# Kernel optimization log

Hardware: AMD Instinct MI355X
Metric: run time of the kernel (lower is better)

## Reference

```python
import jax, jax.numpy as jnp
import numpy as np
import math

QK = 32
IN_DIM = 64
TEXT_DIM = 256


def setup_inputs() -> dict:
    key = jax.random.key(0)
    ks = jax.random.split(key, 12)
    B, C, D, H, W = 2, IN_DIM, 32, 96, 96
    x = jax.random.normal(ks[0], (B, C, D, H, W), dtype=jnp.float32)
    text_emb = jax.random.normal(ks[1], (32, TEXT_DIM), dtype=jnp.float32)
    s = 0.05
    wq = jax.random.normal(ks[2], (QK, C), dtype=jnp.float32) * s
    bq = jax.random.normal(ks[3], (QK,), dtype=jnp.float32) * s
    wk = jax.random.normal(ks[4], (QK, C), dtype=jnp.float32) * s
    bk = jax.random.normal(ks[5], (QK,), dtype=jnp.float32) * s
    wv = jax.random.normal(ks[6], (C, C), dtype=jnp.float32) * s
    bv = jax.random.normal(ks[7], (C,), dtype=jnp.float32) * s
    wt = jax.random.normal(ks[8], (QK, TEXT_DIM), dtype=jnp.float32) * s
    bt = jax.random.normal(ks[9], (QK,), dtype=jnp.float32) * s
    pos_embed = jax.random.normal(ks[10], (1, QK, D, 1, 1), dtype=jnp.float32) * s
    gamma = jax.random.normal(ks[11], (1,), dtype=jnp.float32) * s
    return {"x": x, "text_emb": text_emb, "wq": wq, "bq": bq, "wk": wk,
            "bk": bk, "wv": wv, "bv": bv, "wt": wt, "bt": bt,
            "pos_embed": pos_embed, "gamma": gamma}


def _conv1x1(w, b, x):
    # 1x1x1 Conv3d == channel-mixing matmul: (O,C) x (B,C,D,H,W) -> (B,O,D,H,W)
    return jnp.einsum('oc,bcdhw->bodhw', w, x) + b[None, :, None, None, None]


def reference(x, text_emb, wq, bq, wk, bk, wv, bv, wt, bt, pos_embed, gamma):
    B, C, D, H, W = x.shape
    # text bias: Linear then mean over tokens -> (qk,)
    text_bias = (text_emb @ wt.T + bt).mean(axis=0)
    tb = text_bias[None, :, None, None, None]
    Q = _conv1x1(wq, bq, x) + pos_embed + tb  # (B,qk,D,H,W)
    K = _conv1x1(wk, bk, x) + pos_embed + tb
    V = _conv1x1(wv, bv, x)                   # (B,C,D,H,W)
    scale = math.sqrt(QK)
    # axial attention along D, independent per (b,h,w)
    scores = jnp.einsum('bqdhw,bqehw->bhwde', Q, K) / scale
    attn = jax.nn.softmax(scores, axis=-1)    # (B,H,W,D,D)
    out = jnp.einsum('bhwde,bcehw->bcdhw', attn, V)
    g = jax.nn.sigmoid(gamma[0])
    return g * out + (1.0 - g) * x
```

## Files before the change

kernel.cpp:

```cpp
#include <hip/hip_runtime.h>
#include <hip/hip_bf16.h>

#define B_   2
#define C_   64
#define D_   32
#define H_   96
#define W_   96
#define QK_  32
#define TW_  8
#define HW_  (H_*W_)
#define DHW_ (D_*H_*W_)
#define TDIM_ 256

#define WS_PB   0
#define WS_KB2  1024
#define WS_WQP  2048
#define WS_WKP  3072
#define WS_WVP  4096
#define WS_PBT  6144
#define WS_KBT  7168

typedef __attribute__((ext_vector_type(8))) short short8;
typedef __attribute__((ext_vector_type(4))) float f32x4;

__device__ __forceinline__ uint packbf2(float lo, float hi) {
    uint a = (uint)__bfloat16_as_ushort(__float2bfloat16(lo));
    uint b = (uint)__bfloat16_as_ushort(__float2bfloat16(hi));
    return a | (b << 16);
}

__global__ void prep_kernel(const float* __restrict__ te,
                            const float* __restrict__ wt,
                            const float* __restrict__ bt,
                            const float* __restrict__ bq,
                            const float* __restrict__ bk,
                            const float* __restrict__ wq,
                            const float* __restrict__ wk,
                            const float* __restrict__ wv,
                            const float* __restrict__ pos,
                            float* __restrict__ ws) {
    __shared__ float tm[TDIM_];
    __shared__ float qtb[QK_], ktb[QK_];
    const int t = threadIdx.x;
    float s = 0.f;
    #pragma unroll
    for (int tok = 0; tok < 32; ++tok) s += te[tok*TDIM_ + t];
    tm[t] = s * (1.0f/32.0f);
    __syncthreads();
    if (t < QK_) {
        float acc = bt[t];
        for (int c = 0; c < TDIM_; ++c) acc += wt[t*TDIM_ + c] * tm[c];
        qtb[t] = bq[t] + acc;
        ktb[t] = bk[t] + acc;
    }
    __syncthreads();
    for (int i = t; i < 1024; i += TDIM_) {
        int q = i >> 5, dd = i & 31;
        ws[WS_PB  + i] = qtb[q] + pos[q*32 + dd];
        ws[WS_KB2 + i] = ktb[q] + pos[q*32 + dd];
    }
    for (int i = t; i < 1024; i += TDIM_) {
        int dd = i >> 5, q = i & 31;
        ws[WS_PBT + i] = qtb[q] + pos[q*32 + dd];
        ws[WS_KBT + i] = ktb[q] + pos[q*32 + dd];
    }
    uint* wsu = reinterpret_cast<uint*>(ws);
    for (int i = t; i < 1024; i += TDIM_) {
        int q = i >> 5, cp = i & 31;
        wsu[WS_WQP + i] = packbf2(wq[q*64 + 2*cp], wq[q*64 + 2*cp + 1]);
    }
    for (int i = t; i < 1024; i += TDIM_) {
        int q = i >> 5, cp = i & 31;
        wsu[WS_WKP + i] = packbf2(wk[q*64 + 2*cp], wk[q*64 + 2*cp + 1]);
    }
    for (int i = t; i < 2048; i += TDIM_) {
        int c = i >> 5, cp = i & 31;
        wsu[WS_WVP + i] = packbf2(wv[c*64 + 2*cp], wv[c*64 + 2*cp + 1]);
    }
}

__global__ __launch_bounds__(256, 2)
void attn_main(const float* __restrict__ x,
               const float* __restrict__ bv,
               const float* __restrict__ gm,
               const float* __restrict__ ws,
               float* __restrict__ out) {
    __shared__ uint lds[20480];
    uint* const R_X  = lds;
    uint* const R_QS = lds + 8192;
    uint* const R_KS = lds + 12288;
    uint* const R_V  = lds + 8192;
    uint* const R_AP = lds + 16384;
    uint* const R_O  = lds;

    const uint*  wsu = reinterpret_cast<const uint*>(ws);
    const uint*  wqp = wsu + WS_WQP;
    const uint*  wkp = wsu + WS_WKP;
    const uint*  wvp = wsu + WS_WVP;
    const float* PBT = ws + WS_PBT;
    const float* KBT = ws + WS_KBT;

    const int tid  = threadIdx.x;
    const int lane = tid & 63;
    const int wid  = tid >> 6;
    const int ln   = lane & 15;
    const int lg   = lane >> 4;
    const int d    = tid >> 3;
    const int w    = tid & 7;

    const int bx  = blockIdx.x;
    const int r8  = bx & 7;
    const int q2  = (bx >> 3) & 3;
    const int G   = bx >> 5;
    const int wp_ = G % 3;
    const int hh  = (G / 3) % 12;
    const int b   = G / 36;
    const int h   = hh*8 + r8;
    const int wtile = wp_*4 + q2;

    const int base = b*(C_*DHW_) + d*HW_ + h*W_ + wtile*TW_ + w;

    uint xp[32];
    {
        float xv[64];
        #pragma unroll
        for (int c = 0; c < 64; ++c) xv[c] = x[base + c*DHW_];
        const int key = tid & 7;
        #pragma unroll
        for (int j = 0; j < 8; ++j) {
            uint4 pk;
            pk.x = packbf2(xv[8*j+0], xv[8*j+1]);
            pk.y = packbf2(xv[8*j+2], xv[8*j+3]);
            pk.z = packbf2(xv[8*j+4], xv[8*j+5]);
            pk.w = packbf2(xv[8*j+6], xv[8*j+7]);
            xp[4*j+0] = pk.x; xp[4*j+1] = pk.y;
            xp[4*j+2] = pk.z; xp[4*j+3] = pk.w;
            *reinterpret_cast<uint4*>(R_X + tid*32 + (((j ^ key) & 7) << 2)) = pk;
        }
    }
    __syncthreads();

    {
        uint4 Af[4][2];
        #pragma unroll
        for (int mt = 0; mt < 4; ++mt) {
            const uint* tab = (mt < 2) ? wqp : wkp;
            const int qrow = 16*(mt & 1) + ln;
            #pragma unroll
            for (int kt = 0; kt < 2; ++kt)
                Af[mt][kt] = *reinterpret_cast<const uint4*>(tab + qrow*32 + 16*kt + 4*lg);
        }
        #pragma unroll
        for (int nt = 0; nt < 4; ++nt) {
            const int pos = 16*(4*wid + nt) + ln;
            const int dd  = pos >> 3;
            short8 Bf[2];
            #pragma unroll
            for (int kt = 0; kt < 2; ++kt) {
                uint4 raw = *reinterpret_cast<const uint4*>(
                    R_X + pos*32 + ((((4*kt + lg) ^ (pos & 7)) & 7) << 2));
                Bf[kt] = __builtin_bit_cast(short8, raw);
            }
            #pragma unroll
            for (int mt = 0; mt < 4; ++mt) {
                const float* bt_ = (mt < 2) ? PBT : KBT;
                f32x4 acc = *reinterpret_cast<const f32x4*>(bt_ + dd*32 + 16*(mt & 1) + 4*lg);
                #pragma unroll
                for (int kt = 0; kt < 2; ++kt)
                    acc = __builtin_amdgcn_mfma_f32_16x16x32_bf16(
                        __builtin_bit_cast(short8, Af[mt][kt]), Bf[kt], acc, 0, 0, 0);
                uint p0 = packbf2(acc[0], acc[1]);
                uint p1 = packbf2(acc[2], acc[3]);
                uint* dst = (mt < 2) ? R_QS : R_KS;
                const int s4  = 2*(mt & 1) + (lg >> 1);
                const int off = (((s4 ^ (dd & 3)) & 3) << 2) + 2*(lg & 1);
                *reinterpret_cast<uint2*>(dst + pos*16 + off) = make_uint2(p0, p1);
            }
        }
    }
    __syncthreads();

    {
        const float rsc = 0.17677669529663687f;
        #pragma unroll
        for (int pp = 0; pp < 2; ++pp) {
            const int wp = 2*wid + pp;
            short8 Aq[2], Bk[2];
            #pragma unroll
            for (int t2 = 0; t2 < 2; ++t2) {
                const int row = (16*t2 + ln)*8 + wp;
                const int off = (((lg ^ (ln & 3)) & 3) << 2);
                uint4 rq = *reinterpret_cast<const uint4*>(R_QS + row*16 + off);
                uint4 rk = *reinterpret_cast<const uint4*>(R_KS + row*16 + off);
                Aq[t2] = __builtin_bit_cast(short8, rq);
                Bk[t2] = __builtin_bit_cast(short8, rk);
            }
            f32x4 sc[2][2];
            #pragma unroll
            for (int mtS = 0; mtS < 2; ++mtS)
                #pragma unroll
                for (int ntS = 0; ntS < 2; ++ntS) {
                    f32x4 z = {0.f, 0.f, 0.f, 0.f};
                    sc[mtS][ntS] = __builtin_amdgcn_mfma_f32_16x16x32_bf16(
                        Aq[mtS], Bk[ntS], z, 0, 0, 0);
                }
            #pragma unroll
            for (int mtS = 0; mtS < 2; ++mtS) {
                #pragma unroll
                for (int r2 = 0; r2 < 4; ++r2) {
                    float m = fmaxf(sc[mtS][0][r2], sc[mtS][1][r2]);
                    #pragma unroll
                    for (int sh = 1; sh <= 8; sh <<= 1) m = fmaxf(m, __shfl_xor(m, sh));
                    float p0 = __expf((sc[mtS][0][r2] - m) * rsc);
                    float p1 = __expf((sc[mtS][1][r2] - m) * rsc);
                    float sm = p0 + p1;
                    #pragma unroll
                    for (int sh = 1; sh <= 8; sh <<= 1) sm += __shfl_xor(sm, sh);
                    const float rs = 1.0f / sm;
                    p0 *= rs; p1 *= rs;
                    const float q0 = __shfl_xor(p0, 1);
                    const float q1 = __shfl_xor(p1, 1);
                    if ((lane & 1) == 0) {
                        const int dd2 = 16*mtS + 4*lg + r2;
                        const int u_  = ln >> 1;
                        const int rowb = (dd2*8 + wp)*16;
                        {
                            const int s3  = (u_ >> 2);
                            const int off = (((s3 ^ (dd2 & 3)) & 3) << 2) + (u_ & 3);
                            R_AP[rowb + off] = packbf2(p0, q0);
                        }
                        {
                            const int s3  = 2 + (u_ >> 2);
                            const int off = (((s3 ^ (dd2 & 3)) & 3) << 2) + (u_ & 3);
                            R_AP[rowb + off] = packbf2(p1, q1);
                        }
                    }
                }
            }
        }
    }
    __syncthreads();

    {
        short8 Bf[4][2];
        #pragma unroll
        for (int nt = 0; nt < 4; ++nt) {
            const int pos = 16*(4*wid + nt) + ln;
            #pragma unroll
            for (int kt = 0; kt < 2; ++kt) {
                uint4 raw = *reinterpret_cast<const uint4*>(
                    R_X + pos*32 + ((((4*kt + lg) ^ (pos & 7)) & 7) << 2));
                Bf[nt][kt] = __builtin_bit_cast(short8, raw);
            }
        }
        #pragma unroll
        for (int mt = 0; mt < 4; ++mt) {
            short8 Av[2];
            #pragma unroll
            for (int kt = 0; kt < 2; ++kt) {
                uint4 raw = *reinterpret_cast<const uint4*>(wvp + (16*mt + ln)*32 + 16*kt + 4*lg);
                Av[kt] = __builtin_bit_cast(short8, raw);
            }
            const f32x4 bini = *reinterpret_cast<const f32x4*>(bv + 16*mt + 4*lg);
            f32x4 a4[4];
            #pragma unroll
            for (int nt = 0; nt < 4; ++nt) {
                a4[nt] = bini;
                #pragma unroll
                for (int kt = 0; kt < 2; ++kt)
                    a4[nt] = __builtin_amdgcn_mfma_f32_16x16x32_bf16(Av[kt], Bf[nt][kt], a4[nt], 0, 0, 0);
            }
            #pragma unroll
            for (int r2 = 0; r2 < 4; ++r2) {
                uint u0, u1, u2, u3;
                { float o = a4[0][r2]; float p = __shfl_xor(o, 8); u0 = packbf2(o, p); }
                { float o = a4[1][r2]; float p = __shfl_xor(o, 8); u1 = packbf2(o, p); }
                { float o = a4[2][r2]; float p = __shfl_xor(o, 8); u2 = packbf2(o, p); }
                { float o = a4[3][r2]; float p = __shfl_xor(o, 8); u3 = packbf2(o, p); }
                if ((lane & 8) == 0) {
                    const int c   = 16*mt + 4*lg + r2;
                    const int wv_ = lane & 7;
                    const int phys = (wid ^ lg ^ (wv_ & 3)) & 3;
                    *reinterpret_cast<uint4*>(R_V + (wv_*64 + c)*16 + (phys << 2)) =
                        make_uint4(u0, u1, u2, u3);
                }
            }
        }
    }
    __syncthreads();

    {
        #pragma unroll
        for (int pp = 0; pp < 2; ++pp) {
            const int wp = 2*wid + pp;
            short8 Bp[2];
            #pragma unroll
            for (int ntF = 0; ntF < 2; ++ntF) {
                uint4 raw = *reinterpret_cast<const uint4*>(
                    R_AP + ((16*ntF + ln)*8 + wp)*16 + (((lg ^ (ln & 3)) & 3) << 2));
                Bp[ntF] = __builtin_bit_cast(short8, raw);
            }
            #pragma unroll
            for (int mtF = 0; mtF < 4; ++mtF) {
                const int c = 16*mtF + ln;
                const int phys = (lg ^ ((ln >> 2) & 3) ^ (wp & 3)) & 3;
                uint4 raw = *reinterpret_cast<const uint4*>(R_V + (wp*64 + c)*16 + (phys << 2));
                const short8 Avf = __builtin_bit_cast(short8, raw);
                #pragma unroll
                for (int ntF = 0; ntF < 2; ++ntF) {
                    f32x4 z = {0.f, 0.f, 0.f, 0.f};
                    f32x4 oa = __builtin_amdgcn_mfma_f32_16x16x32_bf16(Avf, Bp[ntF], z, 0, 0, 0);
                    const uint p0 = packbf2(oa[0], oa[1]);
                    const uint p1 = packbf2(oa[2], oa[3]);
                    const int dd3 = 16*ntF + ln;
                    const int s4  = 2*mtF + (lg >> 1);
                    const int off = (((s4 ^ (dd3 & 7)) & 7) << 2) + 2*(lg & 1);
                    *reinterpret_cast<uint2*>(R_O + (dd3*8 + wp)*32 + off) = make_uint2(p0, p1);
                }
            }
        }
    }
    __syncthreads();

    {
        const float gvv = 1.0f / (1.0f + __expf(-gm[0]));
        const float giv = 1.0f - gvv;
        #pragma unroll
        for (int j = 0; j < 8; ++j) {
            uint4 o4 = *reinterpret_cast<const uint4*>(
                R_O + tid*32 + (((j ^ (d & 7)) & 7) << 2));
            const uint os[4] = {o4.x, o4.y, o4.z, o4.w};
            #pragma unroll
            for (int t2 = 0; t2 < 4; ++t2) {
                const uint u  = os[t2];
                const uint xu = xp[4*j + t2];
                const int c   = 8*j + 2*t2;
                const int a0  = base + c*DHW_;
                const float olo = __uint_as_float(u << 16);
                const float ohi = __uint_as_float(u & 0xffff0000u);
                const float xlo = __uint_as_float(xu << 16);
                const float xhi = __uint_as_float(xu & 0xffff0000u);
                out[a0]        = gvv*olo + giv*xlo;
                out[a0 + DHW_] = gvv*ohi + giv*xhi;
            }
        }
    }
}

extern "C" void kernel_launch(void* const* d_in, const int* in_sizes, int n_in,
                              void* d_out, int out_size, void* d_ws, size_t ws_size,
                              hipStream_t stream) {
    const float* x     = (const float*)d_in[0];
    const float* te    = (const float*)d_in[1];
    const float* wq    = (const float*)d_in[2];
    const float* bq    = (const float*)d_in[3];
    const float* wk    = (const float*)d_in[4];
    const float* bk    = (const float*)d_in[5];
    const float* wv    = (const float*)d_in[6];
    const float* bv    = (const float*)d_in[7];
    const float* wt    = (const float*)d_in[8];
    const float* bt    = (const float*)d_in[9];
    const float* pos   = (const float*)d_in[10];
    const float* gamma = (const float*)d_in[11];
    float* out = (float*)d_out;
    float* ws  = (float*)d_ws;

    prep_kernel<<<1, 256, 0, stream>>>(te, wt, bt, bq, bk, wq, wk, wv, pos, ws);

    const int nblk = B_ * H_ * (W_/TW_);
    attn_main<<<nblk, 256, 0, stream>>>(x, bv, gamma, ws, out);
}
```

Baseline: 367.0 us.

## Remap LDS positions per wave so middle stages sync without block barriers

Shared-memory positions are renumbered as P = w*32 + d, so each wave owns whole w-columns through the Q/K projection, scores/softmax, V projection and P·V stages. Three of the four __syncthreads between those stages become per-wave s_waitcnt lgkmcnt(0), and V and O are written into per-wave chunks, with O overwriting that wave's V chunk in place. The 32-register xp copy of x is dropped and re-read from LDS in the epilogue, which lowers register pressure. The trade-off is more complex swizzle indexing, a correctness dependence on strict wave-local data ownership, and extra LDS reads in the epilogue.

```diff
diff --git a/kernel.cpp b/kernel.cpp
--- a/kernel.cpp
+++ b/kernel.cpp
@@ -89,9 +89,7 @@
     uint* const R_X  = lds;
     uint* const R_QS = lds + 8192;
     uint* const R_KS = lds + 12288;
-    uint* const R_V  = lds + 8192;
     uint* const R_AP = lds + 16384;
-    uint* const R_O  = lds;
 
     const uint*  wsu = reinterpret_cast<const uint*>(ws);
     const uint*  wqp = wsu + WS_WQP;
@@ -120,12 +118,12 @@
 
     const int base = b*(C_*DHW_) + d*HW_ + h*W_ + wtile*TW_ + w;
 
-    uint xp[32];
     {
         float xv[64];
         #pragma unroll
         for (int c = 0; c < 64; ++c) xv[c] = x[base + c*DHW_];
-        const int key = tid & 7;
+        const int P0  = w*32 + d;
+        const int key = ((P0 >> 5) ^ P0) & 7;
         #pragma unroll
         for (int j = 0; j < 8; ++j) {
             uint4 pk;
@@ -133,52 +131,49 @@
             pk.y = packbf2(xv[8*j+2], xv[8*j+3]);
             pk.z = packbf2(xv[8*j+4], xv[8*j+5]);
             pk.w = packbf2(xv[8*j+6], xv[8*j+7]);
-            xp[4*j+0] = pk.x; xp[4*j+1] = pk.y;
-            xp[4*j+2] = pk.z; xp[4*j+3] = pk.w;
-            *reinterpret_cast<uint4*>(R_X + tid*32 + (((j ^ key) & 7) << 2)) = pk;
-        }
+            *reinterpret_cast<uint4*>(R_X + P0*32 + (((j ^ key) & 7) << 2)) = pk;
+        }
+    }
+    uint4 Af[4][2];
+    #pragma unroll
+    for (int mt = 0; mt < 4; ++mt) {
+        const uint* tab = (mt < 2) ? wqp : wkp;
+        const int qrow = 16*(mt & 1) + ln;
+        #pragma unroll
+        for (int kt = 0; kt < 2; ++kt)
+            Af[mt][kt] = *reinterpret_cast<const uint4*>(tab + qrow*32 + 16*kt + 4*lg);
     }
     __syncthreads();
 
-    {
-        uint4 Af[4][2];
+    #pragma unroll
+    for (int nt = 0; nt < 4; ++nt) {
+        const int P    = 16*(4*wid + nt) + ln;
+        const int dd   = P & 31;
+        const int keyX = ((P >> 5) ^ P) & 7;
+        short8 Bf[2];
+        #pragma unroll
+        for (int kt = 0; kt < 2; ++kt) {
+            uint4 raw = *reinterpret_cast<const uint4*>(
+                R_X + P*32 + ((((4*kt + lg) ^ keyX) & 7) << 2));
+            Bf[kt] = __builtin_bit_cast(short8, raw);
+        }
+        const int k3 = (P ^ (P >> 2)) & 3;
         #pragma unroll
         for (int mt = 0; mt < 4; ++mt) {
-            const uint* tab = (mt < 2) ? wqp : wkp;
-            const int qrow = 16*(mt & 1) + ln;
+            const float* bt_ = (mt < 2) ? PBT : KBT;
+            f32x4 acc = *reinterpret_cast<const f32x4*>(bt_ + dd*32 + 16*(mt & 1) + 4*lg);
             #pragma unroll
             for (int kt = 0; kt < 2; ++kt)
-                Af[mt][kt] = *reinterpret_cast<const uint4*>(tab + qrow*32 + 16*kt + 4*lg);
-        }
-        #pragma unroll
-        for (int nt = 0; nt < 4; ++nt) {
-            const int pos = 16*(4*wid + nt) + ln;
-            const int dd  = pos >> 3;
-            short8 Bf[2];
-            #pragma unroll
-            for (int kt = 0; kt < 2; ++kt) {
-                uint4 raw = *reinterpret_cast<const uint4*>(
-                    R_X + pos*32 + ((((4*kt + lg) ^ (pos & 7)) & 7) << 2));
-                Bf[kt] = __builtin_bit_cast(short8, raw);
-            }
-            #pragma unroll
-            for (int mt = 0; mt < 4; ++mt) {
-                const float* bt_ = (mt < 2) ? PBT : KBT;
-                f32x4 acc = *reinterpret_cast<const f32x4*>(bt_ + dd*32 + 16*(mt & 1) + 4*lg);
-                #pragma unroll
-                for (int kt = 0; kt < 2; ++kt)
-                    acc = __builtin_amdgcn_mfma_f32_16x16x32_bf16(
-                        __builtin_bit_cast(short8, Af[mt][kt]), Bf[kt], acc, 0, 0, 0);
-                uint p0 = packbf2(acc[0], acc[1]);
-                uint p1 = packbf2(acc[2], acc[3]);
-                uint* dst = (mt < 2) ? R_QS : R_KS;
-                const int s4  = 2*(mt & 1) + (lg >> 1);
-                const int off = (((s4 ^ (dd & 3)) & 3) << 2) + 2*(lg & 1);
-                *reinterpret_cast<uint2*>(dst + pos*16 + off) = make_uint2(p0, p1);
-            }
-        }
-    }
-    __syncthreads();
+                acc = __builtin_amdgcn_mfma_f32_16x16x32_bf16(
+                    __builtin_bit_cast(short8, Af[mt][kt]), Bf[kt], acc, 0, 0, 0);
+            uint p0 = packbf2(acc[0], acc[1]);
+            uint p1 = packbf2(acc[2], acc[3]);
+            uint* dst = (mt < 2) ? R_QS : R_KS;
+            const int off = (((2*(mt & 1) + (lg >> 1)) ^ k3) & 3)*4 + 2*(lg & 1);
+            *reinterpret_cast<uint2*>(dst + P*16 + off) = make_uint2(p0, p1);
+        }
+    }
+    asm volatile("s_waitcnt lgkmcnt(0)" ::: "memory");
 
     {
         const float rsc = 0.17677669529663687f;
@@ -188,10 +183,11 @@
             short8 Aq[2], Bk[2];
             #pragma unroll
             for (int t2 = 0; t2 < 2; ++t2) {
-                const int row = (16*t2 + ln)*8 + wp;
-                const int off = (((lg ^ (ln & 3)) & 3) << 2);
-                uint4 rq = *reinterpret_cast<const uint4*>(R_QS + row*16 + off);
-                uint4 rk = *reinterpret_cast<const uint4*>(R_KS + row*16 + off);
+                const int P  = 32*wp + 16*t2 + ln;
+                const int k3 = (P ^ (P >> 2)) & 3;
+                const int off = ((lg ^ k3) & 3) << 2;
+                uint4 rq = *reinterpret_cast<const uint4*>(R_QS + P*16 + off);
+                uint4 rk = *reinterpret_cast<const uint4*>(R_KS + P*16 + off);
                 Aq[t2] = __builtin_bit_cast(short8, rq);
                 Bk[t2] = __builtin_bit_cast(short8, rk);
             }
@@ -222,35 +218,37 @@
                     const float q1 = __shfl_xor(p1, 1);
                     if ((lane & 1) == 0) {
                         const int dd2 = 16*mtS + 4*lg + r2;
+                        const int k3a = (dd2 ^ (dd2 >> 2)) & 3;
                         const int u_  = ln >> 1;
-                        const int rowb = (dd2*8 + wp)*16;
+                        uint* rowb = R_AP + (32*wp + dd2)*16;
                         {
                             const int s3  = (u_ >> 2);
-                            const int off = (((s3 ^ (dd2 & 3)) & 3) << 2) + (u_ & 3);
-                            R_AP[rowb + off] = packbf2(p0, q0);
+                            const int off = (((s3 ^ k3a) & 3) << 2) + (u_ & 3);
+                            rowb[off] = packbf2(p0, q0);
                         }
                         {
                             const int s3  = 2 + (u_ >> 2);
-                            const int off = (((s3 ^ (dd2 & 3)) & 3) << 2) + (u_ & 3);
-                            R_AP[rowb + off] = packbf2(p1, q1);
+                            const int off = (((s3 ^ k3a) & 3) << 2) + (u_ & 3);
+                            rowb[off] = packbf2(p1, q1);
                         }
                     }
                 }
             }
         }
     }
-    __syncthreads();
-
-    {
-        short8 Bf[4][2];
+    asm volatile("s_waitcnt lgkmcnt(0)" ::: "memory");
+
+    {
+        short8 Bf3[4][2];
         #pragma unroll
         for (int nt = 0; nt < 4; ++nt) {
-            const int pos = 16*(4*wid + nt) + ln;
+            const int P    = 16*(4*wid + nt) + ln;
+            const int keyX = ((P >> 5) ^ P) & 7;
             #pragma unroll
             for (int kt = 0; kt < 2; ++kt) {
                 uint4 raw = *reinterpret_cast<const uint4*>(
-                    R_X + pos*32 + ((((4*kt + lg) ^ (pos & 7)) & 7) << 2));
-                Bf[nt][kt] = __builtin_bit_cast(short8, raw);
+                    R_X + P*32 + ((((4*kt + lg) ^ keyX) & 7) << 2));
+                Bf3[nt][kt] = __builtin_bit_cast(short8, raw);
             }
         }
         #pragma unroll
@@ -268,54 +266,66 @@
                 a4[nt] = bini;
                 #pragma unroll
                 for (int kt = 0; kt < 2; ++kt)
-                    a4[nt] = __builtin_amdgcn_mfma_f32_16x16x32_bf16(Av[kt], Bf[nt][kt], a4[nt], 0, 0, 0);
+                    a4[nt] = __builtin_amdgcn_mfma_f32_16x16x32_bf16(Av[kt], Bf3[nt][kt], a4[nt], 0, 0, 0);
             }
             #pragma unroll
             for (int r2 = 0; r2 < 4; ++r2) {
-                uint u0, u1, u2, u3;
-                { float o = a4[0][r2]; float p = __shfl_xor(o, 8); u0 = packbf2(o, p); }
-                { float o = a4[1][r2]; float p = __shfl_xor(o, 8); u1 = packbf2(o, p); }
-                { float o = a4[2][r2]; float p = __shfl_xor(o, 8); u2 = packbf2(o, p); }
-                { float o = a4[3][r2]; float p = __shfl_xor(o, 8); u3 = packbf2(o, p); }
-                if ((lane & 8) == 0) {
-                    const int c   = 16*mt + 4*lg + r2;
-                    const int wv_ = lane & 7;
-                    const int phys = (wid ^ lg ^ (wv_ & 3)) & 3;
-                    *reinterpret_cast<uint4*>(R_V + (wv_*64 + c)*16 + (phys << 2)) =
-                        make_uint4(u0, u1, u2, u3);
+                const int c    = 16*mt + 4*lg + r2;
+                const int keyV = (c ^ (c >> 2)) & 3;
+                #pragma unroll
+                for (int nt = 0; nt < 4; ++nt) {
+                    float o = a4[nt][r2];
+                    float p = __shfl_xor(o, 1);
+                    uint pk  = packbf2(o, p);
+                    uint pk2 = __shfl_xor(pk, 2);
+                    if ((lane & 3) == 0) {
+                        const int u0  = 8*(nt & 1) + (ln >> 1);
+                        const int off = ((((u0 >> 2) ^ keyV) & 3) << 2) + (u0 & 3);
+                        uint* vb = lds + 8192 + (nt >> 1)*4096 + wid*1024 + c*16;
+                        *reinterpret_cast<uint2*>(vb + off) = make_uint2(pk, pk2);
+                    }
                 }
             }
         }
     }
-    __syncthreads();
+    asm volatile("s_waitcnt lgkmcnt(0)" ::: "memory");
 
     {
         #pragma unroll
         for (int pp = 0; pp < 2; ++pp) {
             const int wp = 2*wid + pp;
+            uint* const vchunk = lds + 8192 + pp*4096 + wid*1024;
             short8 Bp[2];
             #pragma unroll
             for (int ntF = 0; ntF < 2; ++ntF) {
+                const int dd2 = 16*ntF + ln;
+                const int k3a = (dd2 ^ (dd2 >> 2)) & 3;
                 uint4 raw = *reinterpret_cast<const uint4*>(
-                    R_AP + ((16*ntF + ln)*8 + wp)*16 + (((lg ^ (ln & 3)) & 3) << 2));
+                    R_AP + (32*wp + dd2)*16 + (((lg ^ k3a) & 3) << 2));
                 Bp[ntF] = __builtin_bit_cast(short8, raw);
             }
+            short8 Va[4];
             #pragma unroll
             for (int mtF = 0; mtF < 4; ++mtF) {
-                const int c = 16*mtF + ln;
-                const int phys = (lg ^ ((ln >> 2) & 3) ^ (wp & 3)) & 3;
-                uint4 raw = *reinterpret_cast<const uint4*>(R_V + (wp*64 + c)*16 + (phys << 2));
-                const short8 Avf = __builtin_bit_cast(short8, raw);
+                const int c    = 16*mtF + ln;
+                const int keyV = (c ^ (c >> 2)) & 3;
+                uint4 raw = *reinterpret_cast<const uint4*>(
+                    vchunk + c*16 + (((lg ^ keyV) & 3) << 2));
+                Va[mtF] = __builtin_bit_cast(short8, raw);
+            }
+            #pragma unroll
+            for (int mtF = 0; mtF < 4; ++mtF) {
                 #pragma unroll
                 for (int ntF = 0; ntF < 2; ++ntF) {
                     f32x4 z = {0.f, 0.f, 0.f, 0.f};
-                    f32x4 oa = __builtin_amdgcn_mfma_f32_16x16x32_bf16(Avf, Bp[ntF], z, 0, 0, 0);
+                    f32x4 oa = __builtin_amdgcn_mfma_f32_16x16x32_bf16(Va[mtF], Bp[ntF], z, 0, 0, 0);
                     const uint p0 = packbf2(oa[0], oa[1]);
                     const uint p1 = packbf2(oa[2], oa[3]);
-                    const int dd3 = 16*ntF + ln;
-                    const int s4  = 2*mtF + (lg >> 1);
-                    const int off = (((s4 ^ (dd3 & 7)) & 7) << 2) + 2*(lg & 1);
-                    *reinterpret_cast<uint2*>(R_O + (dd3*8 + wp)*32 + off) = make_uint2(p0, p1);
+                    const int dd3  = 16*ntF + ln;
+                    const int keyO = ((dd3 ^ (dd3 >> 3)) ^ wp) & 7;
+                    const int u0   = 8*mtF + 2*lg;
+                    const int off  = ((((u0 >> 2) ^ keyO) & 7) << 2) + (u0 & 3);
+                    *reinterpret_cast<uint2*>(vchunk + dd3*32 + off) = make_uint2(p0, p1);
                 }
             }
         }
@@ -325,15 +335,20 @@
     {
         const float gvv = 1.0f / (1.0f + __expf(-gm[0]));
         const float giv = 1.0f - gvv;
+        const int P0    = w*32 + d;
+        const int keyX0 = ((P0 >> 5) ^ P0) & 7;
+        const int keyO5 = ((d ^ (d >> 3)) ^ w) & 7;
+        const uint* ochunk = lds + 8192 + (w & 1)*4096 + (w >> 1)*1024 + d*32;
         #pragma unroll
         for (int j = 0; j < 8; ++j) {
-            uint4 o4 = *reinterpret_cast<const uint4*>(
-                R_O + tid*32 + (((j ^ (d & 7)) & 7) << 2));
+            uint4 o4 = *reinterpret_cast<const uint4*>(ochunk + (((j ^ keyO5) & 7) << 2));
+            uint4 x4 = *reinterpret_cast<const uint4*>(R_X + P0*32 + (((j ^ keyX0) & 7) << 2));
             const uint os[4] = {o4.x, o4.y, o4.z, o4.w};
+            const uint xs[4] = {x4.x, x4.y, x4.z, x4.w};
             #pragma unroll
             for (int t2 = 0; t2 < 4; ++t2) {
                 const uint u  = os[t2];
-                const uint xu = xp[4*j + t2];
+                const uint xu = xs[t2];
                 const int c   = 8*j + 2*t2;
                 const int a0  = base + c*DHW_;
                 const float olo = __uint_as_float(u << 16);
```

New measurement: 377.3 us. 2.8% more time.
